# Kernel optimization log

Hardware: AMD Instinct MI355X
Metric: run time of the kernel (lower is better)

Reference implementation:

```python
import jax, jax.numpy as jnp
import numpy as np

V, I, H, OUT = 50000, 512, 1024, 2   # node_size, input_dim, hidden_dim, out_dim
P, L = 256, 64                       # num paths, max path length
NH = 32                              # num attention heads
HD = H // NH


def setup_inputs() -> dict:
    key = jax.random.key(0)
    ks = jax.random.split(key, 10)
    paths = jax.random.randint(ks[0], (P, L), 0, V)          # padded path token ids
    lengths = jax.random.randint(ks[1], (P,), 1, L + 1)       # true path lengths in [1, L]
    g = lambda k, shape, s: jax.random.normal(k, shape, jnp.float32) * s
    return {
        "paths": paths,
        "lengths": lengths,
        "emb_table": g(ks[2], (V, I), 0.1),
        "W_ih": g(ks[3], (4 * H, I), 0.02),
        "W_hh": g(ks[4], (4 * H, H), 0.02),
        "b_ih": jnp.zeros((4 * H,), jnp.float32),
        "b_hh": jnp.zeros((4 * H,), jnp.float32),
        "W_in": g(ks[5], (3 * H, H), 0.02),   # packed q,k,v in_proj (torch layout)
        "b_in": jnp.zeros((3 * H,), jnp.float32),
        "W_out": g(ks[6], (H, H), 0.02),
        "b_out": jnp.zeros((H,), jnp.float32),
        "W_lin": g(ks[7], (OUT, H), 0.02),
        "b_lin": jnp.zeros((OUT,), jnp.float32),
    }


def reference(paths, lengths, emb_table, W_ih, W_hh, b_ih, b_hh,
              W_in, b_in, W_out, b_out, W_lin, b_lin):
    p = paths.shape[0]
    x = emb_table[paths]                 # [P, L, I] (batched embedding of all ragged paths)
    xs = jnp.swapaxes(x, 0, 1)           # [L, P, I] time-major for scan
    b = b_ih + b_hh

    def step(carry, xt):                 # single-layer LSTM, torch gate order i,f,g,o
        h, c = carry
        gates = xt @ W_ih.T + h @ W_hh.T + b          # [P, 4H]
        i_g, f_g, g_g, o_g = jnp.split(gates, 4, axis=-1)
        c = jax.nn.sigmoid(f_g) * c + jax.nn.sigmoid(i_g) * jnp.tanh(g_g)
        h = jax.nn.sigmoid(o_g) * jnp.tanh(c)
        return (h, c), h

    h0 = jnp.zeros((p, H), x.dtype)
    _, hs = jax.lax.scan(step, (h0, h0), xs)          # [L, P, H]
    # final hidden of each path at its true length (equiv. to per-path h_n in the torch loop)
    final_h = hs[lengths - 1, jnp.arange(p)]          # [P, H]
    sum_hidden = final_h[None]                        # [1, P, H]  (seq=1, batch=P)

    # nn.MultiheadAttention(sum_hidden, sum_hidden, sum_hidden), seq_len = 1
    qkv = sum_hidden @ W_in.T + b_in                  # [1, P, 3H]
    q, k, v = jnp.split(qkv, 3, axis=-1)
    qh = q.reshape(1, p, NH, HD)
    kh = k.reshape(1, p, NH, HD)
    vh = v.reshape(1, p, NH, HD)
    scale = 1.0 / np.sqrt(HD).astype(np.float32)
    scores = jnp.einsum('qpnd,kpnd->pnqk', qh * scale, kh)   # [P, NH, 1, 1]
    attn = jax.nn.softmax(scores, axis=-1)
    ctx = jnp.einsum('pnqk,kpnd->qpnd', attn, vh).reshape(1, p, H)
    attn_out = ctx @ W_out.T + b_out                  # [1, P, H]

    # MaxPool2d((P,1)) on (C=1, H=P, W=hidden): max over the P paths
    pooled = jnp.max(attn_out, axis=1, keepdims=True)  # [1, 1, H]
    out = jax.nn.sigmoid(pooled @ W_lin.T + b_lin)     # [1, 1, OUT]
    return out
```

## Files before the change

kernel.cpp:

```cpp
#include <hip/hip_runtime.h>
#include <stdint.h>

typedef unsigned short u16;
typedef unsigned int u32;
typedef __attribute__((ext_vector_type(8))) short s16x8;
typedef __attribute__((ext_vector_type(4))) float f32x4;

#define P_ 256
#define L_ 64
#define IDIM 512
#define H_ 1024
#define PH (P_ * H_)

__device__ __forceinline__ u16 f2bf(float f){union{float f;u32 u;}v;v.f=f;u32 u=v.u;return (u16)((u+0x7FFFu+((u>>16)&1u))>>16);}
__device__ __forceinline__ float sigf(float x){return 1.0f/(1.0f+__expf(-x));}
__device__ __forceinline__ float tanhf_(float x){return 1.0f-2.0f/(__expf(2.0f*x)+1.0f);}

__device__ __forceinline__ s16x8 pack8v(float4 a, float4 b){
  s16x8 r;
  r[0]=(short)f2bf(a.x); r[1]=(short)f2bf(a.y); r[2]=(short)f2bf(a.z); r[3]=(short)f2bf(a.w);
  r[4]=(short)f2bf(b.x); r[5]=(short)f2bf(b.y); r[6]=(short)f2bf(b.z); r[7]=(short)f2bf(b.w);
  return r;
}
__device__ __forceinline__ s16x8 pack8(const float* s){
  return pack8v(*(const float4*)s, *(const float4*)(s+4));
}
__device__ __forceinline__ void st16_coh(u16* addr, s16x8 v){
  asm volatile("global_store_dwordx4 %0, %1, off sc0 sc1" :: "v"(addr), "v"(v) : "memory");
}
__device__ __forceinline__ void st_pair(u16* addr, float hv, int lane){
  u32 b = (u32)f2bf(hv);
  u32 other = __shfl_xor(b, 1);
  if ((lane & 1) == 0) {
    u32 w = b | (other << 16);
    __hip_atomic_store((u32*)addr, w, __ATOMIC_RELAXED, __HIP_MEMORY_SCOPE_AGENT);
  }
}
__device__ __forceinline__ void set_flag(u32* f, u32 v){
  __hip_atomic_store(f, v, __ATOMIC_RELAXED, __HIP_MEMORY_SCOPE_AGENT);
}
__device__ __forceinline__ void poll_flags(u32* fg, u32 target, int wid, int lane){
  if (wid == 0) {
    for (;;) {
      u32 f = __hip_atomic_load(&fg[lane], __ATOMIC_RELAXED, __HIP_MEMORY_SCOPE_AGENT);
      if (__all((int)(f >= target))) break;
      __builtin_amdgcn_s_sleep(1);
    }
  }
  asm volatile("" ::: "memory");
  __syncthreads();
}

__global__ void __launch_bounds__(256, 1)
tagger_net(const int* __restrict__ paths, const int* __restrict__ lengths,
           const float* __restrict__ emb,
           const float* __restrict__ Wih, const float* __restrict__ Whh,
           const float* __restrict__ bih, const float* __restrict__ bhh,
           const float* __restrict__ Win, const float* __restrict__ bin,
           const float* __restrict__ Wout, const float* __restrict__ bout,
           const float* __restrict__ Wlin, const float* __restrict__ blin,
           u16* __restrict__ X, u16* __restrict__ Hbuf,
           u16* __restrict__ vbuf, float* __restrict__ pmax,
           u32* flags, float* __restrict__ out)
{
  __shared__ __align__(16) float S[16384];
  const int tid  = threadIdx.x;
  const int wid  = tid >> 6, lane = tid & 63;
  const int lrow = lane & 15, lgrp = lane >> 4;
  const int bid  = blockIdx.x;
  const int g = bid >> 6, jb = bid & 63;
  const int p0 = g * 64, j0 = jb * 16;
  u32* fgrp = flags + g * 64;
  u32* myflag = fgrp + jb;

  for (int it = 0; it < 16; ++it) {
    int e = (it * 256 + tid) * 8;
    int row = e >> 9, col = e & 511;
    int tok = paths[(p0 + row) * L_ + jb];
    const float* s = emb + (size_t)tok * IDIM + col;
    float4 a = *(const float4*)s, b4 = *(const float4*)(s + 4);
    st16_coh(X + ((size_t)jb * P_ + p0 + row) * IDIM + col, pack8v(a, b4));
  }
#pragma unroll
  for (int i = 0; i < 2; ++i) {
    int idx = tid * 2 + i;
    int row = idx >> 3, cp = idx & 7;
    __hip_atomic_store((u32*)&Hbuf[(size_t)(p0 + row) * H_ + j0 + cp * 2], 0u,
                       __ATOMIC_RELAXED, __HIP_MEMORY_SCOPE_AGENT);
  }
  __syncthreads();
  if (tid == 0) set_flag(myflag, 1u);

  s16x8 breg[12][4];
#pragma unroll
  for (int i = 0; i < 12; ++i) {
    const int k = (wid + 4 * i) * 32 + lgrp * 8;
#pragma unroll
    for (int fn = 0; fn < 4; ++fn) {
      const int n = fn * H_ + j0 + lrow;
      const float* src = (k < IDIM) ? (Wih + (size_t)n * IDIM + k)
                                    : (Whh + (size_t)n * H_ + (k - IDIM));
      breg[i][fn] = pack8(src);
    }
  }

  const int prow = p0 + wid * 16 + lgrp * 4;
  int lenr[4]; float biasv[4];
#pragma unroll
  for (int r2 = 0; r2 < 4; ++r2) lenr[r2] = lengths[prow + r2];
#pragma unroll
  for (int fn = 0; fn < 4; ++fn) {
    int n = fn * H_ + j0 + lrow;
    biasv[fn] = bih[n] + bhh[n];
  }
  float cst[4] = {0.f,0.f,0.f,0.f}, hst[4] = {0.f,0.f,0.f,0.f};

  poll_flags(fgrp, 1u, wid, lane);

  const size_t aX = (size_t)(p0 + lrow) * IDIM + lgrp * 8;
  const size_t aH = (size_t)(p0 + lrow) * H_   + lgrp * 8;

  s16x8 fx[4][4];
#define LOADX(T) do { \
    const u16* Xt_ = X + (size_t)(T) * (P_ * IDIM) + aX; \
    _Pragma("unroll") \
    for (int i_ = 0; i_ < 4; ++i_) { \
      const int k0_ = wid * 32 + i_ * 128; \
      _Pragma("unroll") \
      for (int fm_ = 0; fm_ < 4; ++fm_) \
        fx[i_][fm_] = *(const s16x8*)(Xt_ + (size_t)fm_ * (16 * IDIM) + k0_); \
    } } while (0)

  LOADX(0);

  for (int t = 0; t < L_; ++t) {
    const u16* Hr = Hbuf + (size_t)t * PH;
    u16*       Hw = Hbuf + (size_t)(t + 1) * PH;

    f32x4 acc[4][4];
#pragma unroll
    for (int a = 0; a < 4; ++a)
#pragma unroll
      for (int b = 0; b < 4; ++b)
#pragma unroll
        for (int e = 0; e < 4; ++e) acc[a][b][e] = 0.0f;

#pragma unroll
    for (int i = 0; i < 4; ++i)
#pragma unroll
      for (int fm = 0; fm < 4; ++fm)
#pragma unroll
        for (int fn = 0; fn < 4; ++fn)
          acc[fm][fn] = __builtin_amdgcn_mfma_f32_16x16x32_bf16(fx[i][fm], breg[i][fn], acc[fm][fn], 0, 0, 0);

    poll_flags(fgrp, (u32)(t + 1), wid, lane);

    const u16* Hp = Hr + aH;
#pragma unroll
    for (int half = 0; half < 2; ++half) {
      s16x8 fh[4][4];
#pragma unroll
      for (int i = 0; i < 4; ++i) {
        const int kh = wid * 32 + (half * 4 + i) * 128;
#pragma unroll
        for (int fm = 0; fm < 4; ++fm)
          fh[i][fm] = *(const s16x8*)(Hp + (size_t)fm * (16 * H_) + kh);
      }
#pragma unroll
      for (int i = 0; i < 4; ++i)
#pragma unroll
        for (int fm = 0; fm < 4; ++fm)
#pragma unroll
          for (int fn = 0; fn < 4; ++fn)
            acc[fm][fn] = __builtin_amdgcn_mfma_f32_16x16x32_bf16(fh[i][fm], breg[4 + half * 4 + i][fn], acc[fm][fn], 0, 0, 0);
    }

    const int tp1 = (t < L_ - 1) ? (t + 1) : (L_ - 1);
    LOADX(tp1);

#pragma unroll
    for (int fm = 0; fm < 4; ++fm)
#pragma unroll
      for (int fn = 0; fn < 4; ++fn)
        *(f32x4*)&S[((wid * 16) + fm * 4 + fn) * 256 + lane * 4] = acc[fm][fn];
    __syncthreads();
    f32x4 red[4];
#pragma unroll
    for (int fn = 0; fn < 4; ++fn) {
      red[fn] = *(const f32x4*)&S[(wid * 4 + fn) * 256 + lane * 4];
#pragma unroll
      for (int w = 1; w < 4; ++w)
        red[fn] += *(const f32x4*)&S[(w * 16 + wid * 4 + fn) * 256 + lane * 4];
    }

#pragma unroll
    for (int r2 = 0; r2 < 4; ++r2) {
      if (t < lenr[r2]) {
        float gi = red[0][r2] + biasv[0];
        float gf = red[1][r2] + biasv[1];
        float gg = red[2][r2] + biasv[2];
        float go = red[3][r2] + biasv[3];
        float cn = sigf(gf) * cst[r2] + sigf(gi) * tanhf_(gg);
        cst[r2] = cn;
        hst[r2] = sigf(go) * tanhf_(cn);
      }
      st_pair(&Hw[(size_t)(prow + r2) * H_ + j0 + lrow], hst[r2], lane);
    }
    __syncthreads();
    if (tid == 0) set_flag(myflag, (u32)(t + 2));
  }

  const u16* hfin = Hbuf + (size_t)L_ * PH;
  poll_flags(fgrp, 65u, wid, lane);

  {
    f32x4 acc2[4];
#pragma unroll
    for (int a = 0; a < 4; ++a)
#pragma unroll
      for (int e = 0; e < 4; ++e) acc2[a][e] = 0.0f;
    const u16* hp = hfin + aH;
    const float* wv = Win + (size_t)(2 * H_ + j0 + lrow) * H_;
#pragma unroll
    for (int ic = 0; ic < 8; ++ic) {
      const int k0 = wid * 256 + ic * 32;
      s16x8 fbv = pack8(wv + k0 + lgrp * 8);
#pragma unroll
      for (int fm = 0; fm < 4; ++fm) {
        s16x8 fav = *(const s16x8*)(hp + (size_t)fm * (16 * H_) + k0);
        acc2[fm] = __builtin_amdgcn_mfma_f32_16x16x32_bf16(fav, fbv, acc2[fm], 0, 0, 0);
      }
    }
#pragma unroll
    for (int fm = 0; fm < 4; ++fm)
      *(f32x4*)&S[(wid * 4 + fm) * 256 + lane * 4] = acc2[fm];
    __syncthreads();
    f32x4 rv = *(const f32x4*)&S[(wid) * 256 + lane * 4];
#pragma unroll
    for (int w = 1; w < 4; ++w)
      rv += *(const f32x4*)&S[(w * 4 + wid) * 256 + lane * 4];
    float bvj = bin[2 * H_ + j0 + lrow];
#pragma unroll
    for (int r2 = 0; r2 < 4; ++r2)
      st_pair(&vbuf[(size_t)(prow + r2) * H_ + j0 + lrow], rv[r2] + bvj, lane);
  }
  __syncthreads();
  if (tid == 0) set_flag(myflag, 66u);
  poll_flags(fgrp, 66u, wid, lane);

  {
    f32x4 acc2[4];
#pragma unroll
    for (int a = 0; a < 4; ++a)
#pragma unroll
      for (int e = 0; e < 4; ++e) acc2[a][e] = 0.0f;
    const u16* vp = vbuf + aH;
    const float* wo = Wout + (size_t)(j0 + lrow) * H_;
#pragma unroll
    for (int ic = 0; ic < 8; ++ic) {
      const int k0 = wid * 256 + ic * 32;
      s16x8 fbv = pack8(wo + k0 + lgrp * 8);
#pragma unroll
      for (int fm = 0; fm < 4; ++fm) {
        s16x8 fav = *(const s16x8*)(vp + (size_t)fm * (16 * H_) + k0);
        acc2[fm] = __builtin_amdgcn_mfma_f32_16x16x32_bf16(fav, fbv, acc2[fm], 0, 0, 0);
      }
    }
#pragma unroll
    for (int fm = 0; fm < 4; ++fm)
      *(f32x4*)&S[(wid * 4 + fm) * 256 + lane * 4] = acc2[fm];
    __syncthreads();
    f32x4 rv = *(const f32x4*)&S[(wid) * 256 + lane * 4];
#pragma unroll
    for (int w = 1; w < 4; ++w)
      rv += *(const f32x4*)&S[(w * 4 + wid) * 256 + lane * 4];
    float bo = bout[j0 + lrow];
    float m = fmaxf(fmaxf(rv[0], rv[1]), fmaxf(rv[2], rv[3])) + bo;
    __syncthreads();
    S[(wid * 4 + lgrp) * 16 + lrow] = m;
    __syncthreads();
    if (tid < 16) {
      float mx = S[tid];
#pragma unroll
      for (int s2 = 1; s2 < 16; ++s2) mx = fmaxf(mx, S[s2 * 16 + tid]);
      __hip_atomic_store(&pmax[(size_t)g * H_ + j0 + tid], mx, __ATOMIC_RELAXED, __HIP_MEMORY_SCOPE_AGENT);
    }
  }
  __syncthreads();
  if (tid == 0) set_flag(myflag, 67u);

  if (bid != 0) return;

  if (wid == 0) {
    for (int g2 = 0; g2 < 4; ++g2) {
      for (;;) {
        u32 f = __hip_atomic_load(&flags[g2 * 64 + lane], __ATOMIC_RELAXED, __HIP_MEMORY_SCOPE_AGENT);
        if (__all((int)(f >= 67u))) break;
        __builtin_amdgcn_s_sleep(1);
      }
    }
  }
  asm volatile("" ::: "memory");
  __syncthreads();
  {
    int j4 = tid * 4;
    float s0 = 0.f, s1 = 0.f;
#pragma unroll
    for (int e = 0; e < 4; ++e) {
      float pv = pmax[j4 + e];
#pragma unroll
      for (int gg2 = 1; gg2 < 4; ++gg2) pv = fmaxf(pv, pmax[gg2 * H_ + j4 + e]);
      s0 += pv * Wlin[j4 + e];
      s1 += pv * Wlin[H_ + j4 + e];
    }
    S[tid] = s0; S[256 + tid] = s1;
    __syncthreads();
    for (int s2 = 128; s2 > 0; s2 >>= 1) {
      if (tid < s2) { S[tid] += S[tid + s2]; S[256 + tid] += S[256 + tid + s2]; }
      __syncthreads();
    }
    if (tid == 0) {
      out[0] = sigf(S[0] + blin[0]);
      out[1] = sigf(S[256] + blin[1]);
    }
  }
}

extern "C" void kernel_launch(void* const* d_in, const int* in_sizes, int n_in,
                              void* d_out, int out_size, void* d_ws, size_t ws_size,
                              hipStream_t stream) {
  const int*   paths   = (const int*)d_in[0];
  const int*   lengths = (const int*)d_in[1];
  const float* emb     = (const float*)d_in[2];
  const float* Wih     = (const float*)d_in[3];
  const float* Whh     = (const float*)d_in[4];
  const float* bih     = (const float*)d_in[5];
  const float* bhh     = (const float*)d_in[6];
  const float* Win     = (const float*)d_in[7];
  const float* bin     = (const float*)d_in[8];
  const float* Wout    = (const float*)d_in[9];
  const float* bout    = (const float*)d_in[10];
  const float* Wlin    = (const float*)d_in[11];
  const float* blin    = (const float*)d_in[12];
  float* out = (float*)d_out;

  char* ws = (char*)d_ws;
  u32*   flags  = (u32*)  (ws);
  float* pmax   = (float*)(ws + 4096);
  u16*   X      = (u16*)  (ws + 32768);
  u16*   Hbuf   = (u16*)  (ws + 16810240);
  u16*   vbuf   = (u16*)  (ws + 50888960);

  hipMemsetAsync(flags, 0, 1024, stream);
  tagger_net<<<256, 256, 0, stream>>>(paths, lengths, emb, Wih, Whh, bih, bhh,
                                      Win, bin, Wout, bout, Wlin, blin,
                                      X, Hbuf, vbuf, pmax, flags, out);
}
```

Measured before the change: 632.1 us.

## Split paths into eight 32-row groups and launch 512 persistent blocks

```diff
diff --git a/kernel.cpp b/kernel.cpp
--- a/kernel.cpp
+++ b/kernel.cpp
@@ -11,6 +11,8 @@
 #define IDIM 512
 #define H_ 1024
 #define PH (P_ * H_)
+#define NG 8
+#define GM 32
 
 __device__ __forceinline__ u16 f2bf(float f){union{float f;u32 u;}v;v.f=f;u32 u=v.u;return (u16)((u+0x7FFFu+((u>>16)&1u))>>16);}
 __device__ __forceinline__ float sigf(float x){return 1.0f/(1.0f+__expf(-x));}
@@ -63,17 +65,17 @@
            u16* __restrict__ vbuf, float* __restrict__ pmax,
            u32* flags, float* __restrict__ out)
 {
-  __shared__ __align__(16) float S[16384];
+  __shared__ __align__(16) float S[8192];
   const int tid  = threadIdx.x;
   const int wid  = tid >> 6, lane = tid & 63;
   const int lrow = lane & 15, lgrp = lane >> 4;
   const int bid  = blockIdx.x;
   const int g = bid >> 6, jb = bid & 63;
-  const int p0 = g * 64, j0 = jb * 16;
+  const int p0 = g * GM, j0 = jb * 16;
   u32* fgrp = flags + g * 64;
   u32* myflag = fgrp + jb;
 
-  for (int it = 0; it < 16; ++it) {
+  for (int it = 0; it < 8; ++it) {
     int e = (it * 256 + tid) * 8;
     int row = e >> 9, col = e & 511;
     int tok = paths[(p0 + row) * L_ + jb];
@@ -81,10 +83,8 @@
     float4 a = *(const float4*)s, b4 = *(const float4*)(s + 4);
     st16_coh(X + ((size_t)jb * P_ + p0 + row) * IDIM + col, pack8v(a, b4));
   }
-#pragma unroll
-  for (int i = 0; i < 2; ++i) {
-    int idx = tid * 2 + i;
-    int row = idx >> 3, cp = idx & 7;
+  {
+    int row = tid >> 3, cp = tid & 7;
     __hip_atomic_store((u32*)&Hbuf[(size_t)(p0 + row) * H_ + j0 + cp * 2], 0u,
                        __ATOMIC_RELAXED, __HIP_MEMORY_SCOPE_AGENT);
   }
@@ -104,7 +104,8 @@
     }
   }
 
-  const int prow = p0 + wid * 16 + lgrp * 4;
+  const int fmw = wid & 1;
+  const int prow = p0 + fmw * 16 + lgrp * 4;
   int lenr[4]; float biasv[4];
 #pragma unroll
   for (int r2 = 0; r2 < 4; ++r2) lenr[r2] = lengths[prow + r2];
@@ -120,14 +121,14 @@
   const size_t aX = (size_t)(p0 + lrow) * IDIM + lgrp * 8;
   const size_t aH = (size_t)(p0 + lrow) * H_   + lgrp * 8;
 
-  s16x8 fx[4][4];
+  s16x8 fx[4][2];
 #define LOADX(T) do { \
     const u16* Xt_ = X + (size_t)(T) * (P_ * IDIM) + aX; \
     _Pragma("unroll") \
     for (int i_ = 0; i_ < 4; ++i_) { \
       const int k0_ = wid * 32 + i_ * 128; \
       _Pragma("unroll") \
-      for (int fm_ = 0; fm_ < 4; ++fm_) \
+      for (int fm_ = 0; fm_ < 2; ++fm_) \
         fx[i_][fm_] = *(const s16x8*)(Xt_ + (size_t)fm_ * (16 * IDIM) + k0_); \
     } } while (0)
 
@@ -137,9 +138,9 @@
     const u16* Hr = Hbuf + (size_t)t * PH;
     u16*       Hw = Hbuf + (size_t)(t + 1) * PH;
 
-    f32x4 acc[4][4];
-#pragma unroll
-    for (int a = 0; a < 4; ++a)
+    f32x4 acc[2][4];
+#pragma unroll
+    for (int a = 0; a < 2; ++a)
 #pragma unroll
       for (int b = 0; b < 4; ++b)
 #pragma unroll
@@ -148,7 +149,7 @@
 #pragma unroll
     for (int i = 0; i < 4; ++i)
 #pragma unroll
-      for (int fm = 0; fm < 4; ++fm)
+      for (int fm = 0; fm < 2; ++fm)
 #pragma unroll
         for (int fn = 0; fn < 4; ++fn)
           acc[fm][fn] = __builtin_amdgcn_mfma_f32_16x16x32_bf16(fx[i][fm], breg[i][fn], acc[fm][fn], 0, 0, 0);
@@ -158,18 +159,18 @@
     const u16* Hp = Hr + aH;
 #pragma unroll
     for (int half = 0; half < 2; ++half) {
-      s16x8 fh[4][4];
+      s16x8 fh[4][2];
 #pragma unroll
       for (int i = 0; i < 4; ++i) {
         const int kh = wid * 32 + (half * 4 + i) * 128;
 #pragma unroll
-        for (int fm = 0; fm < 4; ++fm)
+        for (int fm = 0; fm < 2; ++fm)
           fh[i][fm] = *(const s16x8*)(Hp + (size_t)fm * (16 * H_) + kh);
       }
 #pragma unroll
       for (int i = 0; i < 4; ++i)
 #pragma unroll
-        for (int fm = 0; fm < 4; ++fm)
+        for (int fm = 0; fm < 2; ++fm)
 #pragma unroll
           for (int fn = 0; fn < 4; ++fn)
             acc[fm][fn] = __builtin_amdgcn_mfma_f32_16x16x32_bf16(fh[i][fm], breg[4 + half * 4 + i][fn], acc[fm][fn], 0, 0, 0);
@@ -179,18 +180,18 @@
     LOADX(tp1);
 
 #pragma unroll
-    for (int fm = 0; fm < 4; ++fm)
+    for (int fm = 0; fm < 2; ++fm)
 #pragma unroll
       for (int fn = 0; fn < 4; ++fn)
-        *(f32x4*)&S[((wid * 16) + fm * 4 + fn) * 256 + lane * 4] = acc[fm][fn];
+        *(f32x4*)&S[((wid * 8) + fm * 4 + fn) * 256 + lane * 4] = acc[fm][fn];
     __syncthreads();
     f32x4 red[4];
 #pragma unroll
     for (int fn = 0; fn < 4; ++fn) {
-      red[fn] = *(const f32x4*)&S[(wid * 4 + fn) * 256 + lane * 4];
+      red[fn] = *(const f32x4*)&S[(fmw * 4 + fn) * 256 + lane * 4];
 #pragma unroll
       for (int w = 1; w < 4; ++w)
-        red[fn] += *(const f32x4*)&S[(w * 16 + wid * 4 + fn) * 256 + lane * 4];
+        red[fn] += *(const f32x4*)&S[(w * 8 + fmw * 4 + fn) * 256 + lane * 4];
     }
 
 #pragma unroll
@@ -204,7 +205,8 @@
         cst[r2] = cn;
         hst[r2] = sigf(go) * tanhf_(cn);
       }
-      st_pair(&Hw[(size_t)(prow + r2) * H_ + j0 + lrow], hst[r2], lane);
+      if (wid < 2)
+        st_pair(&Hw[(size_t)(prow + r2) * H_ + j0 + lrow], hst[r2], lane);
     }
     __syncthreads();
     if (tid == 0) set_flag(myflag, (u32)(t + 2));
@@ -214,9 +216,9 @@
   poll_flags(fgrp, 65u, wid, lane);
 
   {
-    f32x4 acc2[4];
-#pragma unroll
-    for (int a = 0; a < 4; ++a)
+    f32x4 acc2[2];
+#pragma unroll
+    for (int a = 0; a < 2; ++a)
 #pragma unroll
       for (int e = 0; e < 4; ++e) acc2[a][e] = 0.0f;
     const u16* hp = hfin + aH;
@@ -226,32 +228,33 @@
       const int k0 = wid * 256 + ic * 32;
       s16x8 fbv = pack8(wv + k0 + lgrp * 8);
 #pragma unroll
-      for (int fm = 0; fm < 4; ++fm) {
+      for (int fm = 0; fm < 2; ++fm) {
         s16x8 fav = *(const s16x8*)(hp + (size_t)fm * (16 * H_) + k0);
         acc2[fm] = __builtin_amdgcn_mfma_f32_16x16x32_bf16(fav, fbv, acc2[fm], 0, 0, 0);
       }
     }
 #pragma unroll
-    for (int fm = 0; fm < 4; ++fm)
-      *(f32x4*)&S[(wid * 4 + fm) * 256 + lane * 4] = acc2[fm];
-    __syncthreads();
-    f32x4 rv = *(const f32x4*)&S[(wid) * 256 + lane * 4];
+    for (int fm = 0; fm < 2; ++fm)
+      *(f32x4*)&S[(wid * 2 + fm) * 256 + lane * 4] = acc2[fm];
+    __syncthreads();
+    f32x4 rv = *(const f32x4*)&S[(fmw) * 256 + lane * 4];
 #pragma unroll
     for (int w = 1; w < 4; ++w)
-      rv += *(const f32x4*)&S[(w * 4 + wid) * 256 + lane * 4];
+      rv += *(const f32x4*)&S[(w * 2 + fmw) * 256 + lane * 4];
     float bvj = bin[2 * H_ + j0 + lrow];
-#pragma unroll
-    for (int r2 = 0; r2 < 4; ++r2)
-      st_pair(&vbuf[(size_t)(prow + r2) * H_ + j0 + lrow], rv[r2] + bvj, lane);
+    if (wid < 2)
+#pragma unroll
+      for (int r2 = 0; r2 < 4; ++r2)
+        st_pair(&vbuf[(size_t)(prow + r2) * H_ + j0 + lrow], rv[r2] + bvj, lane);
   }
   __syncthreads();
   if (tid == 0) set_flag(myflag, 66u);
   poll_flags(fgrp, 66u, wid, lane);
 
   {
-    f32x4 acc2[4];
-#pragma unroll
-    for (int a = 0; a < 4; ++a)
+    f32x4 acc2[2];
+#pragma unroll
+    for (int a = 0; a < 2; ++a)
 #pragma unroll
       for (int e = 0; e < 4; ++e) acc2[a][e] = 0.0f;
     const u16* vp = vbuf + aH;
@@ -261,19 +264,19 @@
       const int k0 = wid * 256 + ic * 32;
       s16x8 fbv = pack8(wo + k0 + lgrp * 8);
 #pragma unroll
-      for (int fm = 0; fm < 4; ++fm) {
+      for (int fm = 0; fm < 2; ++fm) {
         s16x8 fav = *(const s16x8*)(vp + (size_t)fm * (16 * H_) + k0);
         acc2[fm] = __builtin_amdgcn_mfma_f32_16x16x32_bf16(fav, fbv, acc2[fm], 0, 0, 0);
       }
     }
 #pragma unroll
-    for (int fm = 0; fm < 4; ++fm)
-      *(f32x4*)&S[(wid * 4 + fm) * 256 + lane * 4] = acc2[fm];
-    __syncthreads();
-    f32x4 rv = *(const f32x4*)&S[(wid) * 256 + lane * 4];
+    for (int fm = 0; fm < 2; ++fm)
+      *(f32x4*)&S[(wid * 2 + fm) * 256 + lane * 4] = acc2[fm];
+    __syncthreads();
+    f32x4 rv = *(const f32x4*)&S[(fmw) * 256 + lane * 4];
 #pragma unroll
     for (int w = 1; w < 4; ++w)
-      rv += *(const f32x4*)&S[(w * 4 + wid) * 256 + lane * 4];
+      rv += *(const f32x4*)&S[(w * 2 + fmw) * 256 + lane * 4];
     float bo = bout[j0 + lrow];
     float m = fmaxf(fmaxf(rv[0], rv[1]), fmaxf(rv[2], rv[3])) + bo;
     __syncthreads();
@@ -292,7 +295,7 @@
   if (bid != 0) return;
 
   if (wid == 0) {
-    for (int g2 = 0; g2 < 4; ++g2) {
+    for (int g2 = 0; g2 < NG; ++g2) {
       for (;;) {
         u32 f = __hip_atomic_load(&flags[g2 * 64 + lane], __ATOMIC_RELAXED, __HIP_MEMORY_SCOPE_AGENT);
         if (__all((int)(f >= 67u))) break;
@@ -309,7 +312,7 @@
     for (int e = 0; e < 4; ++e) {
       float pv = pmax[j4 + e];
 #pragma unroll
-      for (int gg2 = 1; gg2 < 4; ++gg2) pv = fmaxf(pv, pmax[gg2 * H_ + j4 + e]);
+      for (int gg2 = 1; gg2 < NG; ++gg2) pv = fmaxf(pv, pmax[gg2 * H_ + j4 + e]);
       s0 += pv * Wlin[j4 + e];
       s1 += pv * Wlin[H_ + j4 + e];
     }
@@ -347,12 +350,12 @@
   char* ws = (char*)d_ws;
   u32*   flags  = (u32*)  (ws);
   float* pmax   = (float*)(ws + 4096);
-  u16*   X      = (u16*)  (ws + 32768);
-  u16*   Hbuf   = (u16*)  (ws + 16810240);
-  u16*   vbuf   = (u16*)  (ws + 50888960);
-
-  hipMemsetAsync(flags, 0, 1024, stream);
-  tagger_net<<<256, 256, 0, stream>>>(paths, lengths, emb, Wih, Whh, bih, bhh,
+  u16*   X      = (u16*)  (ws + 65536);
+  u16*   Hbuf   = (u16*)  (ws + 16842752);
+  u16*   vbuf   = (u16*)  (ws + 50921472);
+
+  hipMemsetAsync(flags, 0, 2048, stream);
+  tagger_net<<<512, 256, 0, stream>>>(paths, lengths, emb, Wih, Whh, bih, bhh,
                                       Win, bin, Wout, bout, Wlin, blin,
                                       X, Hbuf, vbuf, pmax, flags, out);
 }
```

After: 1.229 ms. 94.5% more time.
